# Performance work log

Hardware: AMD Instinct MI355X
Metric: run time of the kernel (lower is better)

## Reference

```python
import jax, jax.numpy as jnp
import numpy as np

D_MODEL = 1024
N_HEADS = 16
HEAD_DIM = D_MODEL // N_HEADS  # 64
D_STATE = 128
D_FF = 4 * D_MODEL
EPS = 1e-6


def rmsnorm(x, w):
    xf = x.astype(jnp.float32)
    var = jnp.mean(xf * xf, axis=-1, keepdims=True)
    return (w * (x * jax.lax.rsqrt(var + EPS))).astype(x.dtype)


def setup_inputs() -> dict:
    key = jax.random.key(0)
    ks = jax.random.split(key, 24)
    B, S = 2, 2048
    inv = lambda n: 1.0 / np.sqrt(n)
    inp = {
        "x": jax.random.normal(ks[0], (B, S, D_MODEL), jnp.float32),
        "attn_mask": jnp.triu(jnp.ones((S, S), jnp.bool_), k=1),  # True = masked (causal)
        "norm1_w": jnp.ones((D_MODEL,), jnp.float32),
        "norm2_w": jnp.ones((D_MODEL,), jnp.float32),
        "norm3_w": jnp.ones((D_MODEL,), jnp.float32),
        "mlpn_w": jnp.ones((D_MODEL,), jnp.float32),
        # projections stored [in, out]; torch Linear y = x @ W.T
        "wq": jax.random.normal(ks[1], (D_MODEL, D_MODEL), jnp.float32) * inv(D_MODEL),
        "wk": jax.random.normal(ks[2], (D_MODEL, D_MODEL), jnp.float32) * inv(D_MODEL),
        "wv": jax.random.normal(ks[3], (D_MODEL, D_MODEL), jnp.float32) * inv(D_MODEL),
        "wo": jax.random.normal(ks[4], (D_MODEL, D_MODEL), jnp.float32) * inv(D_MODEL),
        "qs_w1": jax.random.normal(ks[5], (HEAD_DIM, D_STATE), jnp.float32) * inv(HEAD_DIM),
        "qs_b1": jnp.zeros((D_STATE,), jnp.float32),
        "qs_w2": jax.random.normal(ks[6], (D_STATE, HEAD_DIM), jnp.float32) * inv(D_STATE),
        "qs_b2": jnp.zeros((HEAD_DIM,), jnp.float32),
        "ks_w1": jax.random.normal(ks[7], (HEAD_DIM, D_STATE), jnp.float32) * inv(HEAD_DIM),
        "ks_b1": jnp.zeros((D_STATE,), jnp.float32),
        "ks_w2": jax.random.normal(ks[8], (D_STATE, HEAD_DIM), jnp.float32) * inv(D_STATE),
        "ks_b2": jnp.zeros((HEAD_DIM,), jnp.float32),
        "fc1_w": jax.random.normal(ks[9], (D_MODEL, D_FF), jnp.float32) * inv(D_MODEL),
        "fc1_b": jnp.zeros((D_FF,), jnp.float32),
        "fc2_w": jax.random.normal(ks[10], (D_FF, D_MODEL), jnp.float32) * inv(D_FF),
        "fc2_b": jnp.zeros((D_MODEL,), jnp.float32),
        "gate_w": jax.random.normal(ks[11], (D_MODEL, D_FF), jnp.float32) * inv(D_MODEL),
        "gate_b": jnp.zeros((D_FF,), jnp.float32),
    }
    return inp


def _attention(h, attn_mask, wq, wk, wv, wo,
               qs_w1, qs_b1, qs_w2, qs_b2, ks_w1, ks_b1, ks_w2, ks_b2):
    B, S, _ = h.shape
    q = (h @ wq).reshape(B, S, N_HEADS, HEAD_DIM)
    k = (h @ wk).reshape(B, S, N_HEADS, HEAD_DIM)
    v = (h @ wv).reshape(B, S, N_HEADS, HEAD_DIM)
    # per-head SiLU-MLP residual transform; weights shared across heads -> vectorized
    q = jax.nn.silu(q @ qs_w1 + qs_b1) @ qs_w2 + qs_b2 + q
    k = jax.nn.silu(k @ ks_w1 + ks_b1) @ ks_w2 + ks_b2 + k
    scale = HEAD_DIM ** -0.5
    scores = jnp.einsum('bqhd,bkhd->bhqk', q, k) * scale
    scores = jnp.where(attn_mask[None, None, :, :], -jnp.inf, scores)
    attn = jax.nn.softmax(scores, axis=-1)
    out = jnp.einsum('bhqk,bkhd->bqhd', attn, v).reshape(B, S, D_MODEL)
    return out @ wo


def reference(x, attn_mask, norm1_w, norm2_w, norm3_w, mlpn_w,
              wq, wk, wv, wo,
              qs_w1, qs_b1, qs_w2, qs_b2, ks_w1, ks_b1, ks_w2, ks_b2,
              fc1_w, fc1_b, fc2_w, fc2_b, gate_w, gate_b):
    # Mamba2Block fallback (mamba_ssm unavailable) is the identity on its input,
    # so each mamba stage is: x = x + RMSNorm(x). Dropout is inference identity.
    x = x + rmsnorm(x, norm1_w)
    x = x + rmsnorm(x, norm2_w)
    h = rmsnorm(x, norm3_w)
    x = x + _attention(h, attn_mask, wq, wk, wv, wo,
                       qs_w1, qs_b1, qs_w2, qs_b2, ks_w1, ks_b1, ks_w2, ks_b2)
    hn = rmsnorm(x, mlpn_w)
    gate = jax.nn.silu(hn @ gate_w + gate_b)
    y = gate * (hn @ fc1_w + fc1_b)
    x = x + (y @ fc2_w + fc2_b)
    return x
```

## Files before the change

kernel.cpp:

```cpp
#include <hip/hip_runtime.h>

typedef unsigned short u16;
typedef unsigned int u32;
typedef __bf16 bf16x8 __attribute__((ext_vector_type(8)));
typedef float f32x4 __attribute__((ext_vector_type(4)));

#define D_MODEL 1024
#define SEQ 2048
#define NB 2
#define NH 16
#define HD 64
#define NTOK (NB * SEQ)
#define NTH (NTOK * NH)
#define LDQ 3072

__device__ __forceinline__ float bf2f(u16 v) { return __uint_as_float(((u32)v) << 16); }
__device__ __forceinline__ u16 f2bf(float f) {
    u32 x = __float_as_uint(f);
    x += 0x7fffu + ((x >> 16) & 1u);
    return (u16)(x >> 16);
}
__device__ __forceinline__ u32 cvtpk(float lo, float hi) {
    u32 r;
    asm("v_cvt_pk_bf16_f32 %0, %1, %2" : "=v"(r) : "v"(lo), "v"(hi));
    return r;
}
__device__ __forceinline__ void unp4(uint2 v, float* f) {
    f[0] = __uint_as_float(v.x << 16);
    f[1] = __uint_as_float(v.x & 0xffff0000u);
    f[2] = __uint_as_float(v.y << 16);
    f[3] = __uint_as_float(v.y & 0xffff0000u);
}

__device__ __forceinline__ void gload_lds(const u16* g, u16* l) {
    __builtin_amdgcn_global_load_lds((__attribute__((address_space(1))) u32*)g,
                                     (__attribute__((address_space(3))) u32*)l, 16, 0, 0);
}

struct CJobs { const void* in[12]; u16* out[12]; int n[12]; };

__global__ __launch_bounds__(256) void convmulti_kernel(CJobs jobs, const u32* __restrict__ w0,
                                                        int* __restrict__ flag) {
    const bool f32 = w0[0] == 0x3F800000u;
    if (blockIdx.x == 0 && blockIdx.y == 0 && threadIdx.x == 0) flag[0] = f32 ? 1 : 0;
    const int j = blockIdx.y;
    const int n = jobs.n[j];
    const float* fb = (const float*)jobs.in[j];
    const u16* ib = (const u16*)jobs.in[j];
    u16* ob = jobs.out[j];
    int i = (blockIdx.x * 256 + threadIdx.x) * 8;
    const int str = gridDim.x * 256 * 8;
    for (; i < n; i += str) {
        u16 v[8];
        if (f32) {
#pragma unroll
            for (int t = 0; t < 8; ++t) v[t] = f2bf(fb[i + t]);
        } else {
            *(uint4*)v = *(const uint4*)(ib + i);
        }
        *(uint4*)(ob + i) = *(uint4*)v;
    }
}

#define TJN 11
struct TJobsA { const void* in[TJN]; u16* out[TJN]; int kd[TJN]; int nd[TJN]; int blk0[TJN]; };

__global__ __launch_bounds__(256) void tconvm_all(TJobsA jobs, const u32* __restrict__ w0) {
    __shared__ float tile[32][33];
    const int bid = blockIdx.x;
    int j = 0;
#pragma unroll
    for (int t = 1; t < TJN; ++t)
        if (bid >= jobs.blk0[t]) j = t;
    const int rel = bid - jobs.blk0[j];
    const int Kd = jobs.kd[j], Nd = jobs.nd[j];
    const int ntx = Nd >> 5;
    const int sh = 31 - __clz(ntx);
    const int k0 = (rel >> sh) * 32;
    const int n0 = (rel & (ntx - 1)) * 32;
    const bool f32 = w0[0] == 0x3F800000u;
    const void* in = jobs.in[j];
    u16* out = jobs.out[j];
    const int tx = threadIdx.x & 31, ty = threadIdx.x >> 5;
#pragma unroll
    for (int kk = ty; kk < 32; kk += 8) {
        const size_t sidx = (size_t)(k0 + kk) * Nd + n0 + tx;
        tile[kk][tx] = f32 ? ((const float*)in)[sidx] : bf2f(((const u16*)in)[sidx]);
    }
    __syncthreads();
#pragma unroll
    for (int nn = ty; nn < 32; nn += 8)
        out[(size_t)(n0 + nn) * Kd + k0 + tx] = f2bf(tile[tx][nn]);
}

__device__ __forceinline__ float block_sum(float v, float* red, int tid) {
#pragma unroll
    for (int off = 32; off; off >>= 1) v += __shfl_xor(v, off, 64);
    if ((tid & 63) == 0) red[tid >> 6] = v;
    __syncthreads();
    v = red[0] + red[1] + red[2] + red[3];
    __syncthreads();
    return v;
}

__global__ __launch_bounds__(256) void norm3_kernel(const u16* __restrict__ X,
                                                    const u16* __restrict__ w1,
                                                    const u16* __restrict__ w2,
                                                    const u16* __restrict__ w3,
                                                    float* __restrict__ X2,
                                                    u16* __restrict__ H) {
    __shared__ float red[4];
    const int row = blockIdx.x, tid = threadIdx.x;
    const int c = tid * 4;
    const size_t base = (size_t)row * D_MODEL + c;
    float x[4], w[4];
    unp4(*reinterpret_cast<const uint2*>(X + base), x);

    float ss = x[0] * x[0] + x[1] * x[1] + x[2] * x[2] + x[3] * x[3];
    ss = block_sum(ss, red, tid);
    float r = rsqrtf(ss * (1.f / D_MODEL) + 1e-6f);
    unp4(*reinterpret_cast<const uint2*>(w1 + c), w);
#pragma unroll
    for (int i = 0; i < 4; ++i) x[i] = x[i] + w[i] * x[i] * r;

    ss = x[0] * x[0] + x[1] * x[1] + x[2] * x[2] + x[3] * x[3];
    ss = block_sum(ss, red, tid);
    r = rsqrtf(ss * (1.f / D_MODEL) + 1e-6f);
    unp4(*reinterpret_cast<const uint2*>(w2 + c), w);
#pragma unroll
    for (int i = 0; i < 4; ++i) x[i] = x[i] + w[i] * x[i] * r;

    *reinterpret_cast<float4*>(X2 + base) = make_float4(x[0], x[1], x[2], x[3]);

    ss = x[0] * x[0] + x[1] * x[1] + x[2] * x[2] + x[3] * x[3];
    ss = block_sum(ss, red, tid);
    r = rsqrtf(ss * (1.f / D_MODEL) + 1e-6f);
    unp4(*reinterpret_cast<const uint2*>(w3 + c), w);
    uint2 hv;
    hv.x = (u32)f2bf(w[0] * x[0] * r) | ((u32)f2bf(w[1] * x[1] * r) << 16);
    hv.y = (u32)f2bf(w[2] * x[2] * r) | ((u32)f2bf(w[3] * x[3] * r) << 16);
    *reinterpret_cast<uint2*>(H + base) = hv;
}

__global__ __launch_bounds__(256) void hn_norm_kernel(const float* __restrict__ X3,
                                                      const u16* __restrict__ w,
                                                      u16* __restrict__ HN) {
    __shared__ float red[4];
    const int row = blockIdx.x, tid = threadIdx.x;
    const int c = tid * 4;
    const size_t base = (size_t)row * D_MODEL + c;
    float4 xv = *reinterpret_cast<const float4*>(X3 + base);
    float x[4] = {xv.x, xv.y, xv.z, xv.w};
    float ss = x[0] * x[0] + x[1] * x[1] + x[2] * x[2] + x[3] * x[3];
    ss = block_sum(ss, red, tid);
    float r = rsqrtf(ss * (1.f / D_MODEL) + 1e-6f);
    float w4[4];
    unp4(*reinterpret_cast<const uint2*>(w + c), w4);
    uint2 hv;
    hv.x = (u32)f2bf(w4[0] * x[0] * r) | ((u32)f2bf(w4[1] * x[1] * r) << 16);
    hv.y = (u32)f2bf(w4[2] * x[2] * r) | ((u32)f2bf(w4[3] * x[3] * r) << 16);
    *reinterpret_cast<uint2*>(HN + base) = hv;
}

__global__ __launch_bounds__(256, 4) void mgemm_kernel(const u16* __restrict__ A,
                                                       const u16* __restrict__ Bt,
                                                       const u16* __restrict__ bias,
                                                       const float* __restrict__ resf,
                                                       const u16* __restrict__ mul,
                                                       void* __restrict__ Cout,
                                                       int M, int N, int K, int act, int outf32,
                                                       const int* __restrict__ oflag) {
    __shared__ u16 As[128 * 64];
    __shared__ u16 Bs[128 * 64];
    const int tid = threadIdx.x;
    const int w = tid >> 6, lane = tid & 63;
    const int quad = lane >> 4, l16 = lane & 15;
    const int m0 = blockIdx.y * 128, n0 = blockIdx.x * 128;
    const int wr = (w >> 1) * 64, wc = (w & 1) * 64;

    const int srow = lane >> 3;
    const int scol = ((lane & 7) ^ srow) * 8;
    const u16* Ar = A + (size_t)(m0 + w * 32 + srow) * K + scol;
    const u16* Br = Bt + (size_t)(n0 + w * 32 + srow) * K + scol;
    const int sl0 = l16 & 7;

    f32x4 acc[4][4] = {};

    for (int k0 = 0; k0 < K; k0 += 64) {
#pragma unroll
        for (int i = 0; i < 4; ++i) {
            gload_lds(Ar + (size_t)(i * 8) * K + k0, &As[(w * 32 + i * 8) * 64]);
            gload_lds(Br + (size_t)(i * 8) * K + k0, &Bs[(w * 32 + i * 8) * 64]);
        }
        __syncthreads();
#pragma unroll
        for (int kk = 0; kk < 2; ++kk) {
            const int slot = ((kk * 4 + quad) ^ sl0) * 8;
            bf16x8 a[4], b[4];
#pragma unroll
            for (int i = 0; i < 4; ++i)
                a[i] = *(const bf16x8*)&As[(wr + i * 16 + l16) * 64 + slot];
#pragma unroll
            for (int j = 0; j < 4; ++j)
                b[j] = *(const bf16x8*)&Bs[(wc + j * 16 + l16) * 64 + slot];
#pragma unroll
            for (int i = 0; i < 4; ++i)
#pragma unroll
                for (int j = 0; j < 4; ++j)
                    acc[i][j] = __builtin_amdgcn_mfma_f32_16x16x32_bf16(a[i], b[j], acc[i][j], 0, 0, 0);
        }
        __syncthreads();
    }

    const bool of32 = oflag ? (oflag[0] != 0) : (outf32 != 0);
#pragma unroll
    for (int j = 0; j < 4; ++j) {
        const int col = n0 + wc + j * 16 + l16;
        const float bv = bias ? bf2f(bias[col]) : 0.f;
#pragma unroll
        for (int i = 0; i < 4; ++i) {
            const int rowb = m0 + wr + i * 16 + quad * 4;
#pragma unroll
            for (int r = 0; r < 4; ++r) {
                float v = acc[i][j][r] + bv;
                const size_t idx = (size_t)(rowb + r) * N + col;
                if (act) v = v / (1.f + __expf(-v));
                if (mul) v *= bf2f(mul[idx]);
                if (resf) v += resf[idx];
                if (of32)
                    ((float*)Cout)[idx] = v;
                else
                    ((u16*)Cout)[idx] = f2bf(v);
            }
        }
    }
}

__global__ __launch_bounds__(256, 2) void qkv2_kernel(const u16* __restrict__ A,
                                                      const u16* __restrict__ Bt,
                                                      u16* __restrict__ C) {
    const int N = 3072, K = 1024;
    __shared__ u16 As[128 * 64];
    __shared__ u16 B0s[128 * 64];
    __shared__ u16 B1s[128 * 64];
    const int tid = threadIdx.x;
    const int w = tid >> 6, lane = tid & 63;
    const int quad = lane >> 4, l16 = lane & 15;
    const int m0 = blockIdx.y * 128, n0 = blockIdx.x * 256;
    const int wr = (w >> 1) * 64, wc = (w & 1) * 64;

    const int srow = lane >> 3;
    const int scol = ((lane & 7) ^ srow) * 8;
    const u16* Ar = A + (size_t)(m0 + w * 32 + srow) * K + scol;
    const u16* B0r = Bt + (size_t)(n0 + w * 32 + srow) * K + scol;
    const u16* B1r = Bt + (size_t)(n0 + 128 + w * 32 + srow) * K + scol;
    const int sl0 = l16 & 7;

    f32x4 acc0[4][4] = {};
    f32x4 acc1[4][4] = {};

    for (int k0 = 0; k0 < K; k0 += 64) {
#pragma unroll
        for (int i = 0; i < 4; ++i) {
            gload_lds(Ar + (size_t)(i * 8) * K + k0, &As[(w * 32 + i * 8) * 64]);
            gload_lds(B0r + (size_t)(i * 8) * K + k0, &B0s[(w * 32 + i * 8) * 64]);
            gload_lds(B1r + (size_t)(i * 8) * K + k0, &B1s[(w * 32 + i * 8) * 64]);
        }
        __syncthreads();
#pragma unroll
        for (int kk = 0; kk < 2; ++kk) {
            const int slot = ((kk * 4 + quad) ^ sl0) * 8;
            bf16x8 a[4], b[4];
#pragma unroll
            for (int i = 0; i < 4; ++i)
                a[i] = *(const bf16x8*)&As[(wr + i * 16 + l16) * 64 + slot];
#pragma unroll
            for (int j = 0; j < 4; ++j)
                b[j] = *(const bf16x8*)&B0s[(wc + j * 16 + l16) * 64 + slot];
#pragma unroll
            for (int i = 0; i < 4; ++i)
#pragma unroll
                for (int j = 0; j < 4; ++j)
                    acc0[i][j] = __builtin_amdgcn_mfma_f32_16x16x32_bf16(a[i], b[j], acc0[i][j], 0, 0, 0);
#pragma unroll
            for (int j = 0; j < 4; ++j)
                b[j] = *(const bf16x8*)&B1s[(wc + j * 16 + l16) * 64 + slot];
#pragma unroll
            for (int i = 0; i < 4; ++i)
#pragma unroll
                for (int j = 0; j < 4; ++j)
                    acc1[i][j] = __builtin_amdgcn_mfma_f32_16x16x32_bf16(a[i], b[j], acc1[i][j], 0, 0, 0);
        }
        __syncthreads();
    }

#pragma unroll
    for (int j = 0; j < 4; ++j) {
        const int col = n0 + wc + j * 16 + l16;
#pragma unroll
        for (int i = 0; i < 4; ++i) {
            const int rowb = m0 + wr + i * 16 + quad * 4;
#pragma unroll
            for (int r = 0; r < 4; ++r) {
                const size_t idx = (size_t)(rowb + r) * N + col;
                C[idx] = f2bf(acc0[i][j][r]);
                C[idx + 128] = f2bf(acc1[i][j][r]);
            }
        }
    }
}

__global__ __launch_bounds__(256, 2) void gatefc1_kernel(const u16* __restrict__ A,
                                                         const u16* __restrict__ Bg,
                                                         const u16* __restrict__ Bf,
                                                         const u16* __restrict__ gbias,
                                                         const u16* __restrict__ fbias,
                                                         u16* __restrict__ G1) {
    const int N = 4096, K = 1024;
    __shared__ u16 As[128 * 64];
    __shared__ u16 Bgs[128 * 64];
    __shared__ u16 Bfs[128 * 64];
    const int tid = threadIdx.x;
    const int w = tid >> 6, lane = tid & 63;
    const int quad = lane >> 4, l16 = lane & 15;
    const int m0 = blockIdx.y * 128, n0 = blockIdx.x * 128;
    const int wr = (w >> 1) * 64, wc = (w & 1) * 64;

    const int srow = lane >> 3;
    const int scol = ((lane & 7) ^ srow) * 8;
    const u16* Ar = A + (size_t)(m0 + w * 32 + srow) * K + scol;
    const u16* Bgr = Bg + (size_t)(n0 + w * 32 + srow) * K + scol;
    const u16* Bfr = Bf + (size_t)(n0 + w * 32 + srow) * K + scol;
    const int sl0 = l16 & 7;

    f32x4 accg[4][4] = {};
    f32x4 accf[4][4] = {};

    for (int k0 = 0; k0 < K; k0 += 64) {
#pragma unroll
        for (int i = 0; i < 4; ++i) {
            gload_lds(Ar + (size_t)(i * 8) * K + k0, &As[(w * 32 + i * 8) * 64]);
            gload_lds(Bgr + (size_t)(i * 8) * K + k0, &Bgs[(w * 32 + i * 8) * 64]);
            gload_lds(Bfr + (size_t)(i * 8) * K + k0, &Bfs[(w * 32 + i * 8) * 64]);
        }
        __syncthreads();
#pragma unroll
        for (int kk = 0; kk < 2; ++kk) {
            const int slot = ((kk * 4 + quad) ^ sl0) * 8;
            bf16x8 a[4], b[4];
#pragma unroll
            for (int i = 0; i < 4; ++i)
                a[i] = *(const bf16x8*)&As[(wr + i * 16 + l16) * 64 + slot];
#pragma unroll
            for (int j = 0; j < 4; ++j)
                b[j] = *(const bf16x8*)&Bgs[(wc + j * 16 + l16) * 64 + slot];
#pragma unroll
            for (int i = 0; i < 4; ++i)
#pragma unroll
                for (int j = 0; j < 4; ++j)
                    accg[i][j] = __builtin_amdgcn_mfma_f32_16x16x32_bf16(a[i], b[j], accg[i][j], 0, 0, 0);
#pragma unroll
            for (int j = 0; j < 4; ++j)
                b[j] = *(const bf16x8*)&Bfs[(wc + j * 16 + l16) * 64 + slot];
#pragma unroll
            for (int i = 0; i < 4; ++i)
#pragma unroll
                for (int j = 0; j < 4; ++j)
                    accf[i][j] = __builtin_amdgcn_mfma_f32_16x16x32_bf16(a[i], b[j], accf[i][j], 0, 0, 0);
        }
        __syncthreads();
    }

#pragma unroll
    for (int j = 0; j < 4; ++j) {
        const int col = n0 + wc + j * 16 + l16;
        const float gb = bf2f(gbias[col]);
        const float fb = bf2f(fbias[col]);
#pragma unroll
        for (int i = 0; i < 4; ++i) {
            const int rowb = m0 + wr + i * 16 + quad * 4;
#pragma unroll
            for (int r = 0; r < 4; ++r) {
                float g = accg[i][j][r] + gb;
                g = g / (1.f + __expf(-g));
                const float f = accf[i][j][r] + fb;
                G1[(size_t)(rowb + r) * N + col] = f2bf(g * f);
            }
        }
    }
}

__global__ __launch_bounds__(256) void mgemm64_kernel(const u16* __restrict__ A,
                                                      const u16* __restrict__ Bt,
                                                      const u16* __restrict__ bias,
                                                      const float* __restrict__ resf,
                                                      const u16* __restrict__ mul,
                                                      void* __restrict__ Cout,
                                                      int M, int N, int K, int act, int outf32,
                                                      const int* __restrict__ oflag) {
    __shared__ u16 As[3][64 * 64];
    __shared__ u16 Bs[3][128 * 64];
    const int tid = threadIdx.x;
    const int w = tid >> 6, lane = tid & 63;
    const int quad = lane >> 4, l16 = lane & 15;
    const int m0 = blockIdx.y * 64, n0 = blockIdx.x * 128;
    const int wr = (w >> 1) * 32, wc = (w & 1) * 64;

    const int srow = lane >> 3;
    const int scol = ((lane & 7) ^ srow) * 8;
    const u16* Ar = A + (size_t)(m0 + w * 16 + srow) * K + scol;
    const u16* Br = Bt + (size_t)(n0 + w * 32 + srow) * K + scol;
    const int sl0 = l16 & 7;

    f32x4 acc[2][4] = {};
    const int nt = K >> 6;

    auto STAGE = [&](int t, int buf) {
        const int k0 = t * 64;
#pragma unroll
        for (int i = 0; i < 2; ++i)
            gload_lds(Ar + (size_t)(i * 8) * K + k0, &As[buf][(w * 16 + i * 8) * 64]);
#pragma unroll
        for (int i = 0; i < 4; ++i)
            gload_lds(Br + (size_t)(i * 8) * K + k0, &Bs[buf][(w * 32 + i * 8) * 64]);
    };
    auto COMPUTE = [&](int buf) {
#pragma unroll
        for (int kk = 0; kk < 2; ++kk) {
            const int slot = ((kk * 4 + quad) ^ sl0) * 8;
            bf16x8 a[2], b[4];
#pragma unroll
            for (int i = 0; i < 2; ++i)
                a[i] = *(const bf16x8*)&As[buf][(wr + i * 16 + l16) * 64 + slot];
#pragma unroll
            for (int j = 0; j < 4; ++j)
                b[j] = *(const bf16x8*)&Bs[buf][(wc + j * 16 + l16) * 64 + slot];
#pragma unroll
            for (int i = 0; i < 2; ++i)
#pragma unroll
                for (int j = 0; j < 4; ++j)
                    acc[i][j] = __builtin_amdgcn_mfma_f32_16x16x32_bf16(a[i], b[j], acc[i][j], 0, 0, 0);
        }
    };

    STAGE(0, 0);
    STAGE(1, 1);
    int cb = 0, sb = 2;
    for (int t = 0; t < nt - 2; ++t) {
        STAGE(t + 2, sb);
        asm volatile("s_waitcnt vmcnt(12)" ::: "memory");
        __builtin_amdgcn_sched_barrier(0);
        __builtin_amdgcn_s_barrier();
        COMPUTE(cb);
        __builtin_amdgcn_s_barrier();
        cb = (cb + 1 == 3) ? 0 : cb + 1;
        sb = (sb + 1 == 3) ? 0 : sb + 1;
    }
    asm volatile("s_waitcnt vmcnt(6)" ::: "memory");
    __builtin_amdgcn_sched_barrier(0);
    __builtin_amdgcn_s_barrier();
    COMPUTE(cb);
    __builtin_amdgcn_s_barrier();
    cb = (cb + 1 == 3) ? 0 : cb + 1;
    asm volatile("s_waitcnt vmcnt(0)" ::: "memory");
    __builtin_amdgcn_sched_barrier(0);
    __builtin_amdgcn_s_barrier();
    COMPUTE(cb);

    const bool of32 = oflag ? (oflag[0] != 0) : (outf32 != 0);
#pragma unroll
    for (int j = 0; j < 4; ++j) {
        const int col = n0 + wc + j * 16 + l16;
        const float bv = bias ? bf2f(bias[col]) : 0.f;
#pragma unroll
        for (int i = 0; i < 2; ++i) {
            const int rowb = m0 + wr + i * 16 + quad * 4;
#pragma unroll
            for (int r = 0; r < 4; ++r) {
                float v = acc[i][j][r] + bv;
                const size_t idx = (size_t)(rowb + r) * N + col;
                if (act) v = v / (1.f + __expf(-v));
                if (mul) v *= bf2f(mul[idx]);
                if (resf) v += resf[idx];
                if (of32)
                    ((float*)Cout)[idx] = v;
                else
                    ((u16*)Cout)[idx] = f2bf(v);
            }
        }
    }
}

__global__ __launch_bounds__(256) void headmlp2_kernel(
    u16* __restrict__ QKV,
    const u16* __restrict__ W1tq, const u16* __restrict__ B1q,
    const u16* __restrict__ W2tq, const u16* __restrict__ B2q,
    const u16* __restrict__ W1tk, const u16* __restrict__ B1k,
    const u16* __restrict__ W2tk, const u16* __restrict__ B2k) {
    __shared__ u16 w1s[128 * 64];
    __shared__ u16 w2s[64 * 128];
    __shared__ u16 Ps[4][16 * 136];
    const int tid = threadIdx.x;
    const bool isk = blockIdx.y != 0;
    u16* base = QKV + (isk ? 1024 : 0);
    const u16* W1t = isk ? W1tk : W1tq;
    const u16* B1 = isk ? B1k : B1q;
    const u16* W2t = isk ? W2tk : W2tq;
    const u16* B2 = isk ? B2k : B2q;

    for (int i = tid * 8; i < 8192; i += 2048) {
        *(uint4*)&w1s[i] = *(const uint4*)&W1t[i];
        *(uint4*)&w2s[i] = *(const uint4*)&W2t[i];
    }
    __syncthreads();

    const int w = tid >> 6, lane = tid & 63;
    const int l16 = lane & 15, quad = lane >> 4;
    const int tok0 = blockIdx.x * 8 + w * 2;
    u16* Pw = &Ps[w][0];

    float b1v[8], b2v[4];
#pragma unroll
    for (int t = 0; t < 8; ++t) b1v[t] = bf2f(B1[t * 16 + l16]);
#pragma unroll
    for (int dd = 0; dd < 4; ++dd) b2v[dd] = bf2f(B2[dd * 16 + l16]);

#pragma unroll
    for (int g = 0; g < 2; ++g) {
        const size_t tbase = (size_t)(tok0 + g) * LDQ;
        const u16* qp = base + tbase + l16 * 64 + quad * 8;
        const bf16x8 aq0 = *(const bf16x8*)qp;
        const bf16x8 aq1 = *(const bf16x8*)(qp + 32);

        f32x4 s[8] = {};
#pragma unroll
        for (int t = 0; t < 8; ++t) {
            const bf16x8 b0 = *(const bf16x8*)&w1s[(t * 16 + l16) * 64 + quad * 8];
            const bf16x8 b1f = *(const bf16x8*)&w1s[(t * 16 + l16) * 64 + 32 + quad * 8];
            s[t] = __builtin_amdgcn_mfma_f32_16x16x32_bf16(aq0, b0, s[t], 0, 0, 0);
            s[t] = __builtin_amdgcn_mfma_f32_16x16x32_bf16(aq1, b1f, s[t], 0, 0, 0);
        }
#pragma unroll
        for (int t = 0; t < 8; ++t)
#pragma unroll
            for (int r = 0; r < 4; ++r) {
                float v = s[t][r] + b1v[t];
                v = v / (1.f + __expf(-v));
                Pw[(quad * 4 + r) * 136 + t * 16 + l16] = f2bf(v);
            }
        bf16x8 ap[4];
#pragma unroll
        for (int kk = 0; kk < 4; ++kk)
            ap[kk] = *(const bf16x8*)&Pw[l16 * 136 + kk * 32 + quad * 8];

        f32x4 o[4] = {};
#pragma unroll
        for (int dd = 0; dd < 4; ++dd)
#pragma unroll
            for (int kk = 0; kk < 4; ++kk) {
                const bf16x8 bw = *(const bf16x8*)&w2s[(dd * 16 + l16) * 128 + kk * 32 + quad * 8];
                o[dd] = __builtin_amdgcn_mfma_f32_16x16x32_bf16(ap[kk], bw, o[dd], 0, 0, 0);
            }
#pragma unroll
        for (int r = 0; r < 4; ++r) {
            u16* outp = base + tbase + (quad * 4 + r) * 64 + l16;
#pragma unroll
            for (int dd = 0; dd < 4; ++dd) {
                const float res = bf2f(outp[dd * 16]);
                outp[dd * 16] = f2bf(o[dd][r] + b2v[dd] + res);
            }
        }
    }
}

__global__ __launch_bounds__(256) void transpose_vperm(const u16* __restrict__ Vin,
                                                       u16* __restrict__ T) {
    __shared__ u16 tile[64][65];
    const int bh = blockIdx.y;
    const int b = bh >> 4, h = bh & 15;
    const int s0 = blockIdx.x * 64;
    const int lane = threadIdx.x & 63, sub = threadIdx.x >> 6;
#pragma unroll
    for (int i = 0; i < 64; i += 4) {
        const int s = s0 + i + sub;
        tile[i + sub][lane] = Vin[(size_t)(b * SEQ + s) * LDQ + h * 64 + lane];
    }
    __syncthreads();
    const int key = (lane & 3) * 16 + (lane >> 2);
#pragma unroll
    for (int i = 0; i < 64; i += 4) {
        const int d = i + sub;
        T[((size_t)(bh * HD + d)) * SEQ + s0 + lane] = tile[key][d];
    }
}

__global__ __launch_bounds__(256) void attn_mfma4_kernel(const u16* __restrict__ QKV,
                                                         const u16* __restrict__ Vt,
                                                         u16* __restrict__ AO) {
    __shared__ u16 Ks[3][64 * 64];
    __shared__ u16 Vs[3][64 * 64];
    __shared__ u16 Ps[4][16 * 72];
    __shared__ float Lred[4][16];
    const int tid = threadIdx.x;
    const int w = tid >> 6, lane = tid & 63;
    const int l16 = lane & 15, quad = lane >> 4;
    const int l7 = l16 & 7;
    const int bh = blockIdx.y, b = bh >> 4, h = bh & 15;

    const u16* Kbh = QKV + 1024 + (size_t)b * SEQ * LDQ + h * 64;
    const u16* Vtbh = Vt + (size_t)bh * HD * SEQ;

    const int srl = lane >> 3, sri = lane & 7;
    auto stage = [&](int c, int buf) {
        const int c0 = c * 64;
#pragma unroll
        for (int qq = 0; qq < 2; ++qq) {
            const int r = w * 16 + qq * 8 + srl;
            const int kb = sri ^ (r & 7);
            gload_lds(Kbh + (size_t)(c0 + r) * LDQ + kb * 8, &Ks[buf][(w * 16 + qq * 8) * 64]);
            gload_lds(Vtbh + (size_t)r * SEQ + c0 + kb * 8, &Vs[buf][(w * 16 + qq * 8) * 64]);
        }
    };

    u16* Pw = &Ps[w][0];

#pragma unroll 1
    for (int pass = 0; pass < 2; ++pass) {
        const int x = pass ? blockIdx.x : (2 * gridDim.x - 1 - blockIdx.x);
        const int qw0 = x * 64 + w * 16;
        const int cmax = x;

        const u16* qp = QKV + (size_t)(b * SEQ + qw0 + l16) * LDQ + h * 64 + quad * 8;
        const bf16x8 aq0 = *(const bf16x8*)qp;
        const bf16x8 aq1 = *(const bf16x8*)(qp + 32);
        __builtin_amdgcn_sched_barrier(0);

        f32x4 o[4] = {};
        float lp[4] = {};

        stage(0, 0);
        if (cmax >= 1) stage(1, 1);
        int cb = 0, sb = 2;

        for (int c = 0; c <= cmax; ++c) {
            if (c + 2 <= cmax) {
                stage(c + 2, sb);
                asm volatile("s_waitcnt vmcnt(8)" ::: "memory");
            } else if (c + 1 <= cmax) {
                asm volatile("s_waitcnt vmcnt(4)" ::: "memory");
            } else {
                asm volatile("s_waitcnt vmcnt(0)" ::: "memory");
            }
            __builtin_amdgcn_sched_barrier(0);
            __builtin_amdgcn_s_barrier();

            const int c0 = c * 64;
            const int buf = cb;

            bf16x8 bk[4][2];
#pragma unroll
            for (int t = 0; t < 4; ++t)
#pragma unroll
                for (int h2 = 0; h2 < 2; ++h2)
                    bk[t][h2] =
                        *(const bf16x8*)&Ks[buf][(t * 16 + l16) * 64 + ((h2 * 4 + quad) ^ l7) * 8];
            f32x4 s[4] = {};
#pragma unroll
            for (int t = 0; t < 4; ++t) {
                s[t] = __builtin_amdgcn_mfma_f32_16x16x32_bf16(aq0, bk[t][0], s[t], 0, 0, 0);
                s[t] = __builtin_amdgcn_mfma_f32_16x16x32_bf16(aq1, bk[t][1], s[t], 0, 0, 0);
            }

            float p[4][4];
            if (c == cmax) {
#pragma unroll
                for (int t = 0; t < 4; ++t)
#pragma unroll
                    for (int r = 0; r < 4; ++r)
                        p[t][r] = (c0 + t * 16 + l16 <= qw0 + quad * 4 + r)
                                      ? __expf(fmaf(s[t][r], 0.125f, -8.f))
                                      : 0.f;
            } else {
#pragma unroll
                for (int t = 0; t < 4; ++t)
#pragma unroll
                    for (int r = 0; r < 4; ++r) p[t][r] = __expf(fmaf(s[t][r], 0.125f, -8.f));
            }
#pragma unroll
            for (int r = 0; r < 4; ++r) lp[r] += (p[0][r] + p[1][r]) + (p[2][r] + p[3][r]);

#pragma unroll
            for (int r = 0; r < 4; ++r) {
                uint2 pv;
                pv.x = cvtpk(p[0][r], p[1][r]);
                pv.y = cvtpk(p[2][r], p[3][r]);
                *(uint2*)&Pw[(quad * 4 + r) * 72 + l16 * 4] = pv;
            }
            const bf16x8 ap0 = *(const bf16x8*)&Pw[l16 * 72 + quad * 8];
            const bf16x8 ap1 = *(const bf16x8*)&Pw[l16 * 72 + 32 + quad * 8];

#pragma unroll
            for (int dd = 0; dd < 4; ++dd) {
                const bf16x8 bv0 = *(const bf16x8*)&Vs[buf][(dd * 16 + l16) * 64 + (quad ^ l7) * 8];
                const bf16x8 bv1 =
                    *(const bf16x8*)&Vs[buf][(dd * 16 + l16) * 64 + ((4 + quad) ^ l7) * 8];
                o[dd] = __builtin_amdgcn_mfma_f32_16x16x32_bf16(bv0, ap0, o[dd], 0, 0, 0);
                o[dd] = __builtin_amdgcn_mfma_f32_16x16x32_bf16(bv1, ap1, o[dd], 0, 0, 0);
            }
            __builtin_amdgcn_s_barrier();
            cb = (cb + 1 == 3) ? 0 : cb + 1;
            sb = (sb + 1 == 3) ? 0 : sb + 1;
        }

#pragma unroll
        for (int off = 1; off < 16; off <<= 1)
#pragma unroll
            for (int r = 0; r < 4; ++r) lp[r] += __shfl_xor(lp[r], off, 64);
        if (l16 == 0) {
#pragma unroll
            for (int r = 0; r < 4; ++r) Lred[w][quad * 4 + r] = lp[r];
        }
        __syncthreads();
        const float inv = 1.f / Lred[w][l16];

        u16* optr = AO + ((size_t)(b * SEQ + qw0 + l16) * NH + h) * HD + quad * 4;
#pragma unroll
        for (int dd = 0; dd < 4; ++dd) {
            uint2 ov;
            ov.x = cvtpk(o[dd][0] * inv, o[dd][1] * inv);
            ov.y = cvtpk(o[dd][2] * inv, o[dd][3] * inv);
            *(uint2*)(optr + dd * 16) = ov;
        }
    }
}

static void mgemm(hipStream_t s, const u16* A, const u16* Bt, const u16* bias, const float* resf,
                  const u16* mul, void* C, int M, int N, int K, int act, int outf32,
                  const int* oflag, int bm) {
    if (bm == 64) {
        dim3 grid(N / 128, M / 64);
        mgemm64_kernel<<<grid, 256, 0, s>>>(A, Bt, bias, resf, mul, C, M, N, K, act, outf32, oflag);
    } else {
        dim3 grid(N / 128, M / 128);
        mgemm_kernel<<<grid, 256, 0, s>>>(A, Bt, bias, resf, mul, C, M, N, K, act, outf32, oflag);
    }
}

extern "C" void kernel_launch(void* const* d_in, const int* in_sizes, int n_in, void* d_out,
                              int out_size, void* d_ws, size_t ws_size, hipStream_t stream) {
    (void)in_sizes; (void)n_in; (void)out_size; (void)ws_size;
    char* ws = (char*)d_ws;
    const size_t MiB = (size_t)1 << 20;

    int* flag = (int*)ws;
    u16* SM = (u16*)(ws + 16384);
    u16* qsw1t = SM + 0;      u16* qsb1c = SM + 8192;
    u16* qsw2t = SM + 16384;  u16* qsb2c = SM + 24576;
    u16* ksw1t = SM + 32768;  u16* ksb1c = SM + 40960;
    u16* ksw2t = SM + 49152;  u16* ksb2c = SM + 57344;
    u16* gatebc = SM + 65536; u16* fc1bc = SM + 73728;
    u16* fc2bc = SM + 81920;
    u16* n1c = SM + 90112; u16* n2c = SM + 91136; u16* n3c = SM + 92160; u16* mlpnc = SM + 93184;

    u16* xc    = (u16*)(ws + 1 * MiB);
    u16* Btqkv = (u16*)(ws + 9 * MiB);
    u16* wot   = (u16*)(ws + 15 * MiB);
    u16* gatet = (u16*)(ws + 17 * MiB);
    u16* fc1t  = (u16*)(ws + 25 * MiB);
    u16* fc2t  = (u16*)(ws + 33 * MiB);
    float* X2  = (float*)(ws + 41 * MiB);
    u16* H     = (u16*)(ws + 57 * MiB);
    u16* QKV   = (u16*)(ws + 65 * MiB);
    u16* Vt    = (u16*)(ws + 57 * MiB);
    u16* AO    = (u16*)(ws + 1 * MiB);
    float* X3  = (float*)(ws + 65 * MiB);
    u16* HN    = (u16*)(ws + 81 * MiB);
    u16* G1    = (u16*)(ws + 89 * MiB);

    const u32* w0 = (const u32*)d_in[2];

    CJobs cj;
    cj.in[0] = d_in[0];  cj.out[0] = xc;     cj.n[0] = NTOK * D_MODEL;
    cj.in[1] = d_in[2];  cj.out[1] = n1c;    cj.n[1] = 1024;
    cj.in[2] = d_in[3];  cj.out[2] = n2c;    cj.n[2] = 1024;
    cj.in[3] = d_in[4];  cj.out[3] = n3c;    cj.n[3] = 1024;
    cj.in[4] = d_in[5];  cj.out[4] = mlpnc;  cj.n[4] = 1024;
    cj.in[5] = d_in[11]; cj.out[5] = qsb1c;  cj.n[5] = 128;
    cj.in[6] = d_in[13]; cj.out[6] = qsb2c;  cj.n[6] = 64;
    cj.in[7] = d_in[15]; cj.out[7] = ksb1c;  cj.n[7] = 128;
    cj.in[8] = d_in[17]; cj.out[8] = ksb2c;  cj.n[8] = 64;
    cj.in[9] = d_in[19]; cj.out[9] = fc1bc;  cj.n[9] = 4096;
    cj.in[10] = d_in[21]; cj.out[10] = fc2bc; cj.n[10] = 1024;
    cj.in[11] = d_in[23]; cj.out[11] = gatebc; cj.n[11] = 4096;
    convmulti_kernel<<<dim3(512, 12), 256, 0, stream>>>(cj, w0, flag);

    TJobsA ta;
    ta.in[0] = d_in[10]; ta.out[0] = qsw1t; ta.kd[0] = 64;   ta.nd[0] = 128;  ta.blk0[0] = 0;
    ta.in[1] = d_in[12]; ta.out[1] = qsw2t; ta.kd[1] = 128;  ta.nd[1] = 64;   ta.blk0[1] = 8;
    ta.in[2] = d_in[14]; ta.out[2] = ksw1t; ta.kd[2] = 64;   ta.nd[2] = 128;  ta.blk0[2] = 16;
    ta.in[3] = d_in[16]; ta.out[3] = ksw2t; ta.kd[3] = 128;  ta.nd[3] = 64;   ta.blk0[3] = 24;
    ta.in[4] = d_in[6];  ta.out[4] = Btqkv;               ta.kd[4] = 1024; ta.nd[4] = 1024; ta.blk0[4] = 32;
    ta.in[5] = d_in[7];  ta.out[5] = Btqkv + 1024 * 1024; ta.kd[5] = 1024; ta.nd[5] = 1024; ta.blk0[5] = 1056;
    ta.in[6] = d_in[8];  ta.out[6] = Btqkv + 2048 * 1024; ta.kd[6] = 1024; ta.nd[6] = 1024; ta.blk0[6] = 2080;
    ta.in[7] = d_in[9];  ta.out[7] = wot;                 ta.kd[7] = 1024; ta.nd[7] = 1024; ta.blk0[7] = 3104;
    ta.in[8] = d_in[22]; ta.out[8] = gatet; ta.kd[8] = 1024; ta.nd[8] = 4096; ta.blk0[8] = 4128;
    ta.in[9] = d_in[18]; ta.out[9] = fc1t;  ta.kd[9] = 1024; ta.nd[9] = 4096; ta.blk0[9] = 8224;
    ta.in[10] = d_in[20]; ta.out[10] = fc2t; ta.kd[10] = 4096; ta.nd[10] = 1024; ta.blk0[10] = 12320;
    tconvm_all<<<16416, 256, 0, stream>>>(ta, w0);

    norm3_kernel<<<NTOK, 256, 0, stream>>>(xc, n1c, n2c, n3c, X2, H);
    qkv2_kernel<<<dim3(3072 / 256, NTOK / 128), 256, 0, stream>>>(H, Btqkv, QKV);
    headmlp2_kernel<<<dim3(NTH / 128, 2), 256, 0, stream>>>(
        QKV, qsw1t, qsb1c, qsw2t, qsb2c, ksw1t, ksb1c, ksw2t, ksb2c);
    transpose_vperm<<<dim3(SEQ / 64, NB * NH), 256, 0, stream>>>(QKV + 2048, Vt);
    attn_mfma4_kernel<<<dim3(SEQ / 128, NB * NH), 256, 0, stream>>>(QKV, Vt, AO);
    mgemm(stream, AO, wot, nullptr, X2, nullptr, X3, NTOK, 1024, 1024, 0, 1, nullptr, 64);
    hn_norm_kernel<<<NTOK, 256, 0, stream>>>(X3, mlpnc, HN);
    gatefc1_kernel<<<dim3(32, 32), 256, 0, stream>>>(HN, gatet, fc1t, gatebc, fc1bc, G1);
    mgemm(stream, G1, fc2t, fc2bc, X3, nullptr, d_out, NTOK, 1024, 4096, 0, 0, flag, 64);
}
```

Baseline: 460.7 us.

## Double-buffer LDS in gate/fc1 GEMM and shrink M tile to 64

The fused gate+fc1 GEMM now uses two LDS buffers so the global-to-LDS loads for the next K tile are issued before computing the current one, with one barrier per iteration instead of two. The M tile drops from 128 to 64 rows, doubling the grid to 2048 blocks and halving accumulator registers per thread. The smaller tile lowers arithmetic intensity, since B tiles are reloaded twice as often, and LDS use per block rises to about 80KB, which may limit blocks per CU. The launch-bounds occupancy hint of 2 is removed.

```diff
diff --git a/kernel.cpp b/kernel.cpp
--- a/kernel.cpp
+++ b/kernel.cpp
@@ -310,65 +310,85 @@
     }
 }
 
-__global__ __launch_bounds__(256, 2) void gatefc1_kernel(const u16* __restrict__ A,
-                                                         const u16* __restrict__ Bg,
-                                                         const u16* __restrict__ Bf,
-                                                         const u16* __restrict__ gbias,
-                                                         const u16* __restrict__ fbias,
-                                                         u16* __restrict__ G1) {
+__global__ __launch_bounds__(256) void gatefc1_kernel(const u16* __restrict__ A,
+                                                      const u16* __restrict__ Bg,
+                                                      const u16* __restrict__ Bf,
+                                                      const u16* __restrict__ gbias,
+                                                      const u16* __restrict__ fbias,
+                                                      u16* __restrict__ G1) {
     const int N = 4096, K = 1024;
-    __shared__ u16 As[128 * 64];
-    __shared__ u16 Bgs[128 * 64];
-    __shared__ u16 Bfs[128 * 64];
+    __shared__ u16 As[2][64 * 64];
+    __shared__ u16 Bgs[2][128 * 64];
+    __shared__ u16 Bfs[2][128 * 64];
     const int tid = threadIdx.x;
     const int w = tid >> 6, lane = tid & 63;
     const int quad = lane >> 4, l16 = lane & 15;
-    const int m0 = blockIdx.y * 128, n0 = blockIdx.x * 128;
-    const int wr = (w >> 1) * 64, wc = (w & 1) * 64;
+    const int m0 = blockIdx.y * 64, n0 = blockIdx.x * 128;
+    const int wr = (w >> 1) * 32, wc = (w & 1) * 64;
 
     const int srow = lane >> 3;
     const int scol = ((lane & 7) ^ srow) * 8;
-    const u16* Ar = A + (size_t)(m0 + w * 32 + srow) * K + scol;
+    const u16* Ar = A + (size_t)(m0 + w * 16 + srow) * K + scol;
     const u16* Bgr = Bg + (size_t)(n0 + w * 32 + srow) * K + scol;
     const u16* Bfr = Bf + (size_t)(n0 + w * 32 + srow) * K + scol;
     const int sl0 = l16 & 7;
 
-    f32x4 accg[4][4] = {};
-    f32x4 accf[4][4] = {};
-
-    for (int k0 = 0; k0 < K; k0 += 64) {
+    f32x4 accg[2][4] = {};
+    f32x4 accf[2][4] = {};
+    const int nt = K >> 6;
+
+    auto STAGE = [&](int t, int buf) {
+        const int k0 = t * 64;
+#pragma unroll
+        for (int i = 0; i < 2; ++i)
+            gload_lds(Ar + (size_t)(i * 8) * K + k0, &As[buf][(w * 16 + i * 8) * 64]);
 #pragma unroll
         for (int i = 0; i < 4; ++i) {
-            gload_lds(Ar + (size_t)(i * 8) * K + k0, &As[(w * 32 + i * 8) * 64]);
-            gload_lds(Bgr + (size_t)(i * 8) * K + k0, &Bgs[(w * 32 + i * 8) * 64]);
-            gload_lds(Bfr + (size_t)(i * 8) * K + k0, &Bfs[(w * 32 + i * 8) * 64]);
-        }
-        __syncthreads();
+            gload_lds(Bgr + (size_t)(i * 8) * K + k0, &Bgs[buf][(w * 32 + i * 8) * 64]);
+            gload_lds(Bfr + (size_t)(i * 8) * K + k0, &Bfs[buf][(w * 32 + i * 8) * 64]);
+        }
+    };
+    auto COMPUTE = [&](int buf) {
 #pragma unroll
         for (int kk = 0; kk < 2; ++kk) {
             const int slot = ((kk * 4 + quad) ^ sl0) * 8;
-            bf16x8 a[4], b[4];
-#pragma unroll
-            for (int i = 0; i < 4; ++i)
-                a[i] = *(const bf16x8*)&As[(wr + i * 16 + l16) * 64 + slot];
+            bf16x8 a[2], b[4];
+#pragma unroll
+            for (int i = 0; i < 2; ++i)
+                a[i] = *(const bf16x8*)&As[buf][(wr + i * 16 + l16) * 64 + slot];
 #pragma unroll
             for (int j = 0; j < 4; ++j)
-                b[j] = *(const bf16x8*)&Bgs[(wc + j * 16 + l16) * 64 + slot];
-#pragma unroll
-            for (int i = 0; i < 4; ++i)
+                b[j] = *(const bf16x8*)&Bgs[buf][(wc + j * 16 + l16) * 64 + slot];
+#pragma unroll
+            for (int i = 0; i < 2; ++i)
 #pragma unroll
                 for (int j = 0; j < 4; ++j)
                     accg[i][j] = __builtin_amdgcn_mfma_f32_16x16x32_bf16(a[i], b[j], accg[i][j], 0, 0, 0);
 #pragma unroll
             for (int j = 0; j < 4; ++j)
-                b[j] = *(const bf16x8*)&Bfs[(wc + j * 16 + l16) * 64 + slot];
-#pragma unroll
-            for (int i = 0; i < 4; ++i)
+                b[j] = *(const bf16x8*)&Bfs[buf][(wc + j * 16 + l16) * 64 + slot];
+#pragma unroll
+            for (int i = 0; i < 2; ++i)
 #pragma unroll
                 for (int j = 0; j < 4; ++j)
                     accf[i][j] = __builtin_amdgcn_mfma_f32_16x16x32_bf16(a[i], b[j], accf[i][j], 0, 0, 0);
         }
-        __syncthreads();
+    };
+
+    STAGE(0, 0);
+    asm volatile("s_waitcnt vmcnt(0)" ::: "memory");
+    __builtin_amdgcn_sched_barrier(0);
+    __builtin_amdgcn_s_barrier();
+    int cur = 0;
+    for (int t = 0; t < nt; ++t) {
+        if (t + 1 < nt) STAGE(t + 1, cur ^ 1);
+        COMPUTE(cur);
+        if (t + 1 < nt) {
+            asm volatile("s_waitcnt vmcnt(0)" ::: "memory");
+            __builtin_amdgcn_sched_barrier(0);
+            __builtin_amdgcn_s_barrier();
+        }
+        cur ^= 1;
     }
 
 #pragma unroll
@@ -377,7 +397,7 @@
         const float gb = bf2f(gbias[col]);
         const float fb = bf2f(fbias[col]);
 #pragma unroll
-        for (int i = 0; i < 4; ++i) {
+        for (int i = 0; i < 2; ++i) {
             const int rowb = m0 + wr + i * 16 + quad * 4;
 #pragma unroll
             for (int r = 0; r < 4; ++r) {
@@ -816,6 +836,6 @@
     attn_mfma4_kernel<<<dim3(SEQ / 128, NB * NH), 256, 0, stream>>>(QKV, Vt, AO);
     mgemm(stream, AO, wot, nullptr, X2, nullptr, X3, NTOK, 1024, 1024, 0, 1, nullptr, 64);
     hn_norm_kernel<<<NTOK, 256, 0, stream>>>(X3, mlpnc, HN);
-    gatefc1_kernel<<<dim3(32, 32), 256, 0, stream>>>(HN, gatet, fc1t, gatebc, fc1bc, G1);
+    gatefc1_kernel<<<dim3(4096 / 128, NTOK / 64), 256, 0, stream>>>(HN, gatet, fc1t, gatebc, fc1bc, G1);
     mgemm(stream, G1, fc2t, fc2bc, X3, nullptr, d_out, NTOK, 1024, 4096, 0, 0, flag, 64);
 }
```

New measurement: 506.3 us. 1.1x slower.
